# Kernel tuning notes

Measured on AMD Instinct MI355X. Metric: run time of the kernel, lower is better.

## Reference

```python
import jax, jax.numpy as jnp
import numpy as np

B, L, N_ELECS, N_HID = 2048, 16, 256, 64
N_SITES = L * L  # 256


def setup_inputs() -> dict:
    key = jax.random.key(0)
    k1, k2, k3 = jax.random.split(key, 3)
    # spin configurations in {-1, +1}: one electron per site at half filling
    x = 2 * jax.random.randint(k1, (B, N_SITES), 0, 2, dtype=jnp.int32) - 1
    orbitals_mf = 0.1 * jax.random.normal(k2, (2 * N_SITES, N_ELECS), dtype=jnp.float32)
    orbitals_hf = 0.1 * jax.random.normal(k3, (2 * N_SITES, N_HID), dtype=jnp.float32)
    return {"x": x, "orbitals_mf": orbitals_mf, "orbitals_hf": orbitals_hf}


def reference(x, orbitals_mf, orbitals_hf):
    # x: (B, N_sites) int in {-1,+1}
    n_sites = x.shape[-1]
    # (2N, n_elecs + n_hid)
    orbitals_full = jnp.concatenate([orbitals_mf, orbitals_hf], axis=1)
    spin_up = (x == 1)   # (B, N)
    spin_dn = (x == -1)  # (B, N)
    mask = jnp.concatenate([spin_up, spin_dn], axis=-1).astype(jnp.int32)  # (B, 2N)
    # top_k over the boolean mask: indices of occupied spin-orbitals,
    # ties (equal values) resolved by lowest index, matching jax.lax.top_k on bools
    _, idx = jax.lax.top_k(mask, n_sites)  # (B, N)
    # gather orbital rows: (B, N, n_elecs + n_hid)
    return orbitals_full[idx, :]
```

## Files before the change

kernel.cpp:

```cpp
#include <hip/hip_runtime.h>


#define NBATCH 2048
#define NS 256
#define NMF 256
#define NHF 64
#define NROW 320

typedef float v4f __attribute__((ext_vector_type(4)));

__global__ __launch_bounds__(256) void gather_orbitals(
    const int* __restrict__ x,
    const float* __restrict__ mf,
    const float* __restrict__ hf,
    float* __restrict__ out)
{
    __shared__ int src[NS];
    __shared__ int wtot[4];

    const int b    = blockIdx.x;
    const int tid  = threadIdx.x;
    const int wave = tid >> 6;
    const int lane = tid & 63;

    const int xv = x[(size_t)b * NS + tid];
    const bool up = (xv == 1);
    const unsigned long long m = __ballot(up);
    const int lane_ex = __popcll(m & ((1ull << lane) - 1ull));
    if (lane == 0) wtot[wave] = __popcll(m);
    __syncthreads();

    int woff = 0, nup = 0;
#pragma unroll
    for (int w = 0; w < 4; ++w) {
        const int c = wtot[w];
        if (w < wave) woff += c;
        nup += c;
    }
    const int upex = woff + lane_ex;
    const int dest = up ? upex : (nup + (tid - upex));
    src[dest] = up ? tid : (NS + tid);
    __syncthreads();

    float* outb = out + (size_t)b * NS * NROW;

#pragma unroll 8
    for (int r = wave; r < NS; r += 4) {
        const int s = src[r];
        const v4f v = ((const v4f*)(mf + (size_t)s * NMF))[lane];
        __builtin_nontemporal_store(v, ((v4f*)(outb + (size_t)r * NROW)) + lane);
    }

    const int r16 = tid >> 4;
    const int l16 = tid & 15;
#pragma unroll 4
    for (int r = r16; r < NS; r += 16) {
        const int s = src[r];
        const v4f v = ((const v4f*)(hf + (size_t)s * NHF))[l16];
        __builtin_nontemporal_store(v, ((v4f*)(outb + (size_t)r * NROW + NMF)) + l16);
    }
}

extern "C" void kernel_launch(void* const* d_in, const int* in_sizes, int n_in,
                              void* d_out, int out_size, void* d_ws, size_t ws_size,
                              hipStream_t stream) {
    const int*   x  = (const int*)d_in[0];
    const float* mf = (const float*)d_in[1];
    const float* hf = (const float*)d_in[2];
    float* out = (float*)d_out;

    gather_orbitals<<<dim3(NBATCH), dim3(256), 0, stream>>>(x, mf, hf, out);
}
```

Measured before the change: 134.3 us.

## Stage orbital column tiles in LDS and loop over batch groups per block

```diff
diff --git a/kernel.cpp b/kernel.cpp
--- a/kernel.cpp
+++ b/kernel.cpp
@@ -1,63 +1,97 @@
 #include <hip/hip_runtime.h>
 
 
-#define NBATCH 2048
 #define NS 256
 #define NMF 256
 #define NHF 64
 #define NROW 320
+#define G 10
+#define CW 32
+#define NBG 51
+#define THREADS 512
 
 typedef float v4f __attribute__((ext_vector_type(4)));
 
-__global__ __launch_bounds__(256) void gather_orbitals(
+__global__ __launch_bounds__(THREADS, 4) void gather_orbitals(
     const int* __restrict__ x,
     const float* __restrict__ mf,
     const float* __restrict__ hf,
     float* __restrict__ out)
 {
-    __shared__ int src[NS];
-    __shared__ int wtot[4];
+    extern __shared__ float smem[];
+    float* orb  = smem;
+    int*   srcs = (int*)(smem + 512 * CW);
+    int*   wtot = srcs + 2 * NS;
 
-    const int b    = blockIdx.x;
+    const int cg = blockIdx.x % G;
+    const int bg = blockIdx.x / G;
+
+    const float* srcp; int pitch, src_col0, out_col0;
+    if (cg < 8) { srcp = mf; pitch = NMF; src_col0 = cg * CW;       out_col0 = cg * CW; }
+    else        { srcp = hf; pitch = NHF; src_col0 = (cg - 8) * CW; out_col0 = NMF + (cg - 8) * CW; }
+
     const int tid  = threadIdx.x;
+    const int half = tid >> 8;
+    const int t    = tid & 255;
     const int wave = tid >> 6;
     const int lane = tid & 63;
 
-    const int xv = x[(size_t)b * NS + tid];
-    const bool up = (xv == 1);
-    const unsigned long long m = __ballot(up);
-    const int lane_ex = __popcll(m & ((1ull << lane) - 1ull));
-    if (lane == 0) wtot[wave] = __popcll(m);
+    {
+        const int gl = tid & 7;
+        const int jr = tid >> 3;
+#pragma unroll
+        for (int i = 0; i < 8; ++i) {
+            const int j = i * 64 + jr;
+            const v4f v = *(const v4f*)(srcp + (size_t)j * pitch + src_col0 + gl * 4);
+#pragma unroll
+            for (int k = 0; k < 4; ++k)
+                orb[(j << 5) + ((gl * 4 + k + j) & 31)] = v[k];
+        }
+    }
     __syncthreads();
 
-    int woff = 0, nup = 0;
+    const int nb     = 40 + (bg < 8);
+    const int bstart = bg * 40 + (bg < 8 ? bg : 8);
+
+    const int li = t & 31;
+    const int r0 = t >> 5;
+
+    for (int ib = 0; ib < nb; ib += 2) {
+        const int  bi    = ib + half;
+        const bool valid = bi < nb;
+        const int  b0    = bstart + bi;
+
+        bool up = false;
+        if (valid) up = (x[(size_t)b0 * NS + t] == 1);
+        const unsigned long long m = __ballot(valid && up);
+        const int lane_ex = __popcll(m & ((1ull << lane) - 1ull));
+        if (lane == 0) wtot[wave] = __popcll(m);
+        __syncthreads();
+        if (valid) {
+            const int wbase = half * 4, wl = wave & 3;
+            int woff = 0, nup = 0;
 #pragma unroll
-    for (int w = 0; w < 4; ++w) {
-        const int c = wtot[w];
-        if (w < wave) woff += c;
-        nup += c;
-    }
-    const int upex = woff + lane_ex;
-    const int dest = up ? upex : (nup + (tid - upex));
-    src[dest] = up ? tid : (NS + tid);
-    __syncthreads();
-
-    float* outb = out + (size_t)b * NS * NROW;
-
+            for (int w = 0; w < 4; ++w) {
+                const int c = wtot[wbase + w];
+                if (w < wl) woff += c;
+                nup += c;
+            }
+            const int upex = woff + lane_ex;
+            const int dest = up ? upex : (nup + (t - upex));
+            srcs[half * NS + dest] = up ? t : (NS + t);
+        }
+        __syncthreads();
+        if (valid) {
+            float* outb = out + (size_t)b0 * NS * NROW + out_col0;
 #pragma unroll 8
-    for (int r = wave; r < NS; r += 4) {
-        const int s = src[r];
-        const v4f v = ((const v4f*)(mf + (size_t)s * NMF))[lane];
-        __builtin_nontemporal_store(v, ((v4f*)(outb + (size_t)r * NROW)) + lane);
-    }
-
-    const int r16 = tid >> 4;
-    const int l16 = tid & 15;
-#pragma unroll 4
-    for (int r = r16; r < NS; r += 16) {
-        const int s = src[r];
-        const v4f v = ((const v4f*)(hf + (size_t)s * NHF))[l16];
-        __builtin_nontemporal_store(v, ((v4f*)(outb + (size_t)r * NROW + NMF)) + l16);
+            for (int p = 0; p < 32; ++p) {
+                const int r = p * 8 + r0;
+                const int s = srcs[half * NS + r];
+                const float v = orb[(s << 5) + ((li + s) & 31)];
+                outb[(size_t)r * NROW + li] = v;
+            }
+        }
+        __syncthreads();
     }
 }
 
@@ -69,5 +103,9 @@
     const float* hf = (const float*)d_in[2];
     float* out = (float*)d_out;
 
-    gather_orbitals<<<dim3(NBATCH), dim3(256), 0, stream>>>(x, mf, hf, out);
+    const int lds_bytes = 512 * CW * 4 + 2 * NS * 4 + 8 * 4;
+    (void)hipFuncSetAttribute((const void*)gather_orbitals,
+                              hipFuncAttributeMaxDynamicSharedMemorySize,
+                              lds_bytes);
+    gather_orbitals<<<dim3(G * NBG), dim3(THREADS), lds_bytes, stream>>>(x, mf, hf, out);
 }
```

Result: slower. 139.1 us (+3.5%).
